# Kernel tuning notes

Hardware: AMD Instinct MI355X
Metric: run time of the kernel (lower is better)

Reference implementation:

```python
import jax, jax.numpy as jnp
import numpy as np

IN_SIZE = 64
NUM_FEATURES = 32
NUM_HEADS = 8
EPS = 1e-5


def setup_inputs() -> dict:
    key = jax.random.key(0)
    ks = jax.random.split(key, 12)
    D, F, Hh = IN_SIZE, NUM_FEATURES, NUM_HEADS
    M = Hh * F  # MLP width = num_heads * num_features
    s = 0.05
    return {
        "x": jax.random.normal(ks[0], (2, D, 48, 48), dtype=jnp.float32),
        # stacked per-head projection weights, stored [in, out]
        "Wq": jax.random.normal(ks[1], (Hh, D, F), dtype=jnp.float32) * s,
        "bq": jax.random.normal(ks[2], (Hh, F), dtype=jnp.float32) * s,
        "Wk": jax.random.normal(ks[3], (Hh, D, F), dtype=jnp.float32) * s,
        "bk": jax.random.normal(ks[4], (Hh, F), dtype=jnp.float32) * s,
        "Wv": jax.random.normal(ks[5], (Hh, D, F), dtype=jnp.float32) * s,
        "bv": jax.random.normal(ks[6], (Hh, F), dtype=jnp.float32) * s,
        "W1": jax.random.normal(ks[7], (M, M), dtype=jnp.float32) * s,
        "b1": jax.random.normal(ks[8], (M,), dtype=jnp.float32) * s,
        "W2": jax.random.normal(ks[9], (M, M), dtype=jnp.float32) * s,
        "b2": jax.random.normal(ks[10], (M,), dtype=jnp.float32) * s,
        "gamma": jnp.ones((M,), dtype=jnp.float32),
        "beta": jnp.zeros((M,), dtype=jnp.float32),
    }


def _inorm_lastdim(y):
    # InstanceNorm1d applied to channels-last tensor: normalizes LAST dim,
    # biased variance, eps=1e-5, no affine.
    mu = jnp.mean(y, axis=-1, keepdims=True)
    var = jnp.mean(jnp.square(y - mu), axis=-1, keepdims=True)
    return (y - mu) / jnp.sqrt(var + EPS)


def reference(x, Wq, bq, Wk, bk, Wv, bv, W1, b1, W2, b2, gamma, beta):
    N, D, H, W = x.shape
    F = NUM_FEATURES
    L = H * W
    flat = jnp.transpose(x, (0, 2, 3, 1)).reshape(N, L, D)  # [N, L, D]

    def proj(Wm, bm):  # Wm [Hh, D, F], bm [Hh, F] -> [Hh, N, L, F]
        y = jnp.einsum('nld,hdf->hnlf', flat, Wm) + bm[:, None, None, :]
        return jax.nn.relu(_inorm_lastdim(y))

    Q = proj(Wq, bq)
    K = proj(Wk, bk)
    V = proj(Wv, bv)

    scores = jnp.einsum('hnlf,hnmf->hnlm', Q, K) / jnp.sqrt(jnp.float32(F))
    # original: F.softmax(scaled) on 3D [N,L,L] -> legacy dim=1 (first L axis)
    att = jax.nn.softmax(scores, axis=2)
    A = jnp.einsum('hnlm,hnmf->hnlf', att, V)  # [Hh, N, L, F]

    heads = jnp.transpose(A, (1, 2, 0, 3)).reshape(N, L, NUM_HEADS * F)
    m = jax.nn.relu(heads @ W1 + b1)
    m = jax.nn.relu(m @ W2 + b2)
    o = _inorm_lastdim(m + heads)
    o = gamma * o + beta  # [N, L, Hh*F]
    return jnp.transpose(o, (0, 2, 1)).reshape(N, NUM_HEADS * F, H, W)
```

## Files before the change

kernel.cpp:

```cpp
#include <hip/hip_runtime.h>
#include <hip/hip_bf16.h>
#include <stdint.h>

#define L_TOT 2304
#define D_IN  64
#define NF    32
#define NH    8
#define NB    2
#define MW    256
#define CHS   8
#define NSTRIP (L_TOT/32)

constexpr float EPSV  = 1e-5f;
constexpr float SCALE2 = 0.2550351f;

typedef __bf16  bf16x8  __attribute__((ext_vector_type(8)));
typedef float   f32x16  __attribute__((ext_vector_type(16)));
typedef float   f32x4   __attribute__((ext_vector_type(4)));

union U32x4BF { uint32_t u[4]; bf16x8 v; };

static __device__ __forceinline__ uint32_t pack_bf16(float a, float b) {
    union { __bf16 h[2]; uint32_t u; } r;
    r.h[0] = (__bf16)a;
    r.h[1] = (__bf16)b;
    return r.u;
}

__global__ __launch_bounds__(256) void k_prep(
    const float* __restrict__ x,
    const float* __restrict__ Wq, const float* __restrict__ Wk, const float* __restrict__ Wv,
    const float* __restrict__ W1, const float* __restrict__ W2,
    __hip_bfloat16* __restrict__ xb, __hip_bfloat16* __restrict__ Wqkvt,
    __hip_bfloat16* __restrict__ W1t, __hip_bfloat16* __restrict__ W2t)
{
    const int job = blockIdx.x;
    const int tx = threadIdx.x & 31, ty = threadIdx.x >> 5;
    __shared__ float t[64][33];

    if (job < 128) {
        const int z = job >> 6;
        const int tt = job & 63;
        const int bi = (tt >> 3) * 32, bj = (tt & 7) * 32;
        const float* src = z ? W2 : W1;
        __hip_bfloat16* dst = z ? W2t : W1t;
        #pragma unroll
        for (int k = 0; k < 4; ++k)
            t[ty + 8 * k][tx] = src[(size_t)(bi + ty + 8 * k) * MW + bj + tx];
        __syncthreads();
        #pragma unroll
        for (int k = 0; k < 4; ++k)
            dst[(size_t)(bj + ty + 8 * k) * MW + bi + tx] =
                __float2bfloat16(t[tx][ty + 8 * k]);
        return;
    }

    const float* src;
    size_t sstride;
    __hip_bfloat16* dst;
    if (job < 152) {
        int j = job - 128;
        int mtx = j >> 3, h = j & 7;
        const float* Wm = mtx == 0 ? Wq : (mtx == 1 ? Wk : Wv);
        src = Wm + (size_t)h * D_IN * NF;
        sstride = NF;
        dst = Wqkvt + (size_t)j * NF * D_IN;
    } else {
        int i = job - 152;
        int n = i / NSTRIP, lt = i % NSTRIP;
        src = x + (size_t)n * D_IN * L_TOT + lt * 32;
        sstride = L_TOT;
        dst = xb + ((size_t)n * L_TOT + lt * 32) * D_IN;
    }
    #pragma unroll
    for (int k = 0; k < 8; ++k)
        t[ty + 8 * k][tx] = src[(size_t)(ty + 8 * k) * sstride + tx];
    __syncthreads();
    #pragma unroll
    for (int k = 0; k < 4; ++k) {
        int col = ty + 8 * k;
        #pragma unroll
        for (int j = 0; j < 2; ++j)
            dst[(size_t)col * D_IN + tx + 32 * j] = __float2bfloat16(t[tx + 32 * j][col]);
    }
}

__global__ __launch_bounds__(512) void k_proj(
    const __hip_bfloat16* __restrict__ xb, const __hip_bfloat16* __restrict__ Wqkvt,
    const float* __restrict__ bq, const float* __restrict__ bk, const float* __restrict__ bv,
    __hip_bfloat16* __restrict__ Qo, __hip_bfloat16* __restrict__ Ko,
    __hip_bfloat16* __restrict__ Vt)
{
    const int ltile = blockIdx.x;
    const int n = blockIdx.y;
    const int mtx = blockIdx.z;
    const int h = threadIdx.x >> 6;
    const int l0 = ltile * 32;
    const int lane = threadIdx.x & 63;
    const int c = lane & 31, hi = lane >> 5;
    const int hn = h * NB + n;

    const bf16x8* xp = reinterpret_cast<const bf16x8*>(
        xb + ((size_t)n * L_TOT + l0 + c) * D_IN);
    bf16x8 xf[4];
    #pragma unroll
    for (int t = 0; t < 4; ++t) xf[t] = xp[2 * t + hi];

    const float* bsp = mtx == 0 ? bq : (mtx == 1 ? bk : bv);

    const bf16x8* wp = reinterpret_cast<const bf16x8*>(
        Wqkvt + ((size_t)(mtx * NH + h) * NF + c) * D_IN);
    f32x16 acc = {};
    #pragma unroll
    for (int t = 0; t < 4; ++t)
        acc = __builtin_amdgcn_mfma_f32_32x32x16_bf16(wp[2 * t + hi], xf[t], acc, 0, 0, 0);

    float bb[16];
    #pragma unroll
    for (int g = 0; g < 4; ++g) {
        float4 t4 = *reinterpret_cast<const float4*>(&bsp[h * NF + 8 * g + 4 * hi]);
        bb[4 * g + 0] = t4.x; bb[4 * g + 1] = t4.y;
        bb[4 * g + 2] = t4.z; bb[4 * g + 3] = t4.w;
    }

    float v[16], s = 0.f, s2 = 0.f;
    #pragma unroll
    for (int r = 0; r < 16; ++r) {
        v[r] = acc[r] + bb[r];
        s += v[r]; s2 += v[r] * v[r];
    }
    s  += __shfl_xor(s, 32, 64);
    s2 += __shfl_xor(s2, 32, 64);
    float mu = s * (1.f / 32);
    float rstd = rsqrtf(s2 * (1.f / 32) - mu * mu + EPSV);
    float y[16];
    #pragma unroll
    for (int r = 0; r < 16; ++r) y[r] = fmaxf((v[r] - mu) * rstd, 0.f);

    if (mtx == 2) {
        #pragma unroll
        for (int r = 0; r < 16; ++r) {
            int f = (r & 3) + 8 * (r >> 2) + 4 * hi;
            Vt[((size_t)(hn * NSTRIP + ltile) * NF + f) * 32 + c] = __float2bfloat16(y[r]);
        }
    } else {
        if (mtx == 0) {
            #pragma unroll
            for (int r = 0; r < 16; ++r) y[r] *= SCALE2;
        }
        uint32_t pk[8];
        #pragma unroll
        for (int q = 0; q < 8; ++q) pk[q] = pack_bf16(y[2 * q], y[2 * q + 1]);
        uint32_t rr[4];
        #pragma unroll
        for (int j = 0; j < 4; ++j)
            rr[j] = (uint32_t)__shfl_xor((int)(hi ? pk[j] : pk[4 + j]), 32, 64);
        uint32_t row[8];
        if (hi == 0) {
            row[0] = pk[0]; row[1] = pk[1]; row[2] = rr[0]; row[3] = rr[1];
            row[4] = pk[2]; row[5] = pk[3]; row[6] = rr[2]; row[7] = rr[3];
        } else {
            row[0] = rr[0]; row[1] = rr[1]; row[2] = pk[4]; row[3] = pk[5];
            row[4] = rr[2]; row[5] = rr[3]; row[6] = pk[6]; row[7] = pk[7];
        }
        __hip_bfloat16* dst = (mtx == 0 ? Qo : Ko)
            + ((size_t)hn * L_TOT + l0 + c) * NF + hi * 16;
        reinterpret_cast<uint4*>(dst)[0] = make_uint4(row[0], row[1], row[2], row[3]);
        reinterpret_cast<uint4*>(dst)[1] = make_uint4(row[4], row[5], row[6], row[7]);
    }
}

__global__ __launch_bounds__(256) void k_stats(
    const __hip_bfloat16* __restrict__ Qb, const __hip_bfloat16* __restrict__ Kb,
    float* __restrict__ zpart)
{
    const int w = threadIdx.x >> 6;
    const int strip = blockIdx.x * 4 + w;
    const int hn = blockIdx.y;
    const int chunk = blockIdx.z;
    const int lane = threadIdx.x & 63;
    const int c = lane & 31, hi = lane >> 5;

    const bf16x8* kp = reinterpret_cast<const bf16x8*>(
        Kb + ((size_t)hn * L_TOT + strip * 32 + c) * NF);
    const bf16x8 kb0 = kp[hi];
    const bf16x8 kb1 = kp[2 + hi];

    float z0 = 0.f, z1 = 0.f, z2 = 0.f, z3 = 0.f;

    for (int it = 0; it < (L_TOT / 32) / CHS; ++it) {
        const int l0 = (chunk * ((L_TOT / 32) / CHS) + it) * 32;
        const bf16x8* qp = reinterpret_cast<const bf16x8*>(
            Qb + ((size_t)hn * L_TOT + l0 + c) * NF);
        f32x16 s16 = {};
        s16 = __builtin_amdgcn_mfma_f32_32x32x16_bf16(qp[hi], kb0, s16, 0, 0, 0);
        s16 = __builtin_amdgcn_mfma_f32_32x32x16_bf16(qp[2 + hi], kb1, s16, 0, 0, 0);
        #pragma unroll
        for (int r = 0; r < 4; ++r) z0 += exp2f(s16[r]);
        #pragma unroll
        for (int r = 4; r < 8; ++r) z1 += exp2f(s16[r]);
        #pragma unroll
        for (int r = 8; r < 12; ++r) z2 += exp2f(s16[r]);
        #pragma unroll
        for (int r = 12; r < 16; ++r) z3 += exp2f(s16[r]);
    }
    float Z = (z0 + z1) + (z2 + z3);
    Z += __shfl_xor(Z, 32, 64);
    if (hi == 0)
        zpart[((size_t)chunk * 16 + hn) * L_TOT + strip * 32 + c] = Z;
}

__global__ __launch_bounds__(256) void k_norm(
    const float* __restrict__ zpart, __hip_bfloat16* __restrict__ Vt)
{
    const int strip = blockIdx.x, hn = blockIdx.y;
    __shared__ float zs[CHS][32];
    __shared__ float zinv_s[32];

    const int cc = threadIdx.x >> 5, p = threadIdx.x & 31;
    zs[cc][p] = zpart[((size_t)cc * 16 + hn) * L_TOT + strip * 32 + p];
    __syncthreads();
    if (threadIdx.x < 32) {
        float Z = 0.f;
        #pragma unroll
        for (int k = 0; k < CHS; ++k) Z += zs[k][threadIdx.x];
        zinv_s[threadIdx.x] = 1.f / Z;
    }
    __syncthreads();

    const int f = threadIdx.x >> 3, mg = (threadIdx.x & 7) * 4;
    __hip_bfloat16* pv = Vt + ((size_t)(hn * NSTRIP + strip) * NF + f) * 32 + mg;
    uint2* p2v = reinterpret_cast<uint2*>(pv);
    union { uint2 u2; __bf16 h[4]; } in, outv;
    in.u2 = *p2v;
    outv.h[0] = (__bf16)((float)in.h[0] * zinv_s[mg + 0]);
    outv.h[1] = (__bf16)((float)in.h[1] * zinv_s[mg + 1]);
    outv.h[2] = (__bf16)((float)in.h[2] * zinv_s[mg + 2]);
    outv.h[3] = (__bf16)((float)in.h[3] * zinv_s[mg + 3]);
    *p2v = outv.u2;
}

static __device__ __forceinline__ void apply_strip(
    int st, int hn, const bf16x8& qb0, const bf16x8& qb1,
    const __hip_bfloat16* __restrict__ Kb, const __hip_bfloat16* __restrict__ Vt,
    int c, int hi, f32x16& acc)
{
    const bf16x8* kp = reinterpret_cast<const bf16x8*>(
        Kb + ((size_t)hn * L_TOT + st * 32 + c) * NF);
    f32x16 s16 = {};
    s16 = __builtin_amdgcn_mfma_f32_32x32x16_bf16(kp[hi], qb0, s16, 0, 0, 0);
    s16 = __builtin_amdgcn_mfma_f32_32x32x16_bf16(kp[2 + hi], qb1, s16, 0, 0, 0);

    float p[16];
    #pragma unroll
    for (int r = 0; r < 16; ++r) p[r] = exp2f(s16[r]);

    uint32_t wp[8];
    #pragma unroll
    for (int q = 0; q < 8; ++q) wp[q] = pack_bf16(p[2 * q], p[2 * q + 1]);

    uint32_t sendA = hi ? wp[0] : wp[2];
    uint32_t sendB = hi ? wp[1] : wp[3];
    uint32_t rA = (uint32_t)__shfl_xor((int)sendA, 32, 64);
    uint32_t rB = (uint32_t)__shfl_xor((int)sendB, 32, 64);
    U32x4BF fragP0;
    fragP0.u[0] = hi ? rA    : wp[0];
    fragP0.u[1] = hi ? rB    : wp[1];
    fragP0.u[2] = hi ? wp[2] : rA;
    fragP0.u[3] = hi ? wp[3] : rB;
    uint32_t sendC = hi ? wp[4] : wp[6];
    uint32_t sendD = hi ? wp[5] : wp[7];
    uint32_t rC = (uint32_t)__shfl_xor((int)sendC, 32, 64);
    uint32_t rD = (uint32_t)__shfl_xor((int)sendD, 32, 64);
    U32x4BF fragP1;
    fragP1.u[0] = hi ? rC    : wp[4];
    fragP1.u[1] = hi ? rD    : wp[5];
    fragP1.u[2] = hi ? wp[6] : rC;
    fragP1.u[3] = hi ? wp[7] : rD;

    const bf16x8* vp = reinterpret_cast<const bf16x8*>(
        Vt + ((size_t)(hn * NSTRIP + st) * NF + c) * 32);
    acc = __builtin_amdgcn_mfma_f32_32x32x16_bf16(fragP0.v, vp[hi], acc, 0, 0, 0);
    acc = __builtin_amdgcn_mfma_f32_32x32x16_bf16(fragP1.v, vp[2 + hi], acc, 0, 0, 0);
}

__global__ __launch_bounds__(512) void k_apply(
    const __hip_bfloat16* __restrict__ Qb, const __hip_bfloat16* __restrict__ Kb,
    const __hip_bfloat16* __restrict__ Vt,
    float* __restrict__ partA)
{
    const int w = threadIdx.x >> 6;
    const int ltile = blockIdx.x;
    const int l0 = ltile * 32;
    const int hn = blockIdx.y;
    const int lane = threadIdx.x & 63;
    const int c = lane & 31, hi = lane >> 5;

    const bf16x8* qp = reinterpret_cast<const bf16x8*>(
        Qb + ((size_t)hn * L_TOT + l0 + c) * NF);
    const bf16x8 qb0 = qp[hi];
    const bf16x8 qb1 = qp[2 + hi];

    f32x16 accA = {}, accB = {};
    const int sbase = w * (NSTRIP / 8);
    #pragma unroll
    for (int it2 = 0; it2 < 4; ++it2) {
        apply_strip(sbase + 2 * it2,     hn, qb0, qb1, Kb, Vt, c, hi, accA);
        apply_strip(sbase + 2 * it2 + 1, hn, qb0, qb1, Kb, Vt, c, hi, accB);
    }
    apply_strip(sbase + 8, hn, qb0, qb1, Kb, Vt, c, hi, accA);

    __shared__ float red[8][16][64];
    #pragma unroll
    for (int r = 0; r < 16; ++r) red[w][r][lane] = accA[r] + accB[r];
    __syncthreads();

    const int n = hn & 1, h = hn >> 1;
    float* outp = partA + ((size_t)(n * L_TOT + l0)) * MW + h * NF + c;
    #pragma unroll
    for (int j = 0; j < 2; ++j) {
        const int r = 2 * w + j;
        float sv = 0.f;
        #pragma unroll
        for (int k = 0; k < 8; ++k) sv += red[k][r][lane];
        const int row = (r & 3) + 8 * (r >> 2) + 4 * hi;
        outp[(size_t)row * MW] = sv;
    }
}

__global__ __launch_bounds__(512) void k_mlp(
    const float* __restrict__ partA,
    const __hip_bfloat16* __restrict__ W1t, const float* __restrict__ b1,
    const __hip_bfloat16* __restrict__ W2t, const float* __restrict__ b2,
    const float* __restrict__ gamma, const float* __restrict__ beta,
    float* __restrict__ out)
{
    const int blk = blockIdx.x;
    const int n  = blk / (L_TOT / 16);
    const int l0 = (blk % (L_TOT / 16)) * 16;
    const int tid = threadIdx.x;
    const int w = tid >> 6, lane = tid & 63;
    const int ar = lane & 15;
    const int kg = lane >> 4;
    const int n0 = w * 32;

    __shared__ __align__(16) char smem[50176];
    float (*hsf)[MW] = reinterpret_cast<float (*)[MW]>(smem);
    __hip_bfloat16 (*hA)[264]  = reinterpret_cast<__hip_bfloat16 (*)[264]>(smem + 16384);
    __hip_bfloat16 (*msb)[264] = reinterpret_cast<__hip_bfloat16 (*)[264]>(smem + 24832);
    float (*ys)[MW] = reinterpret_cast<float (*)[MW]>(smem + 33280);
    float (*rs)[4]  = reinterpret_cast<float (*)[4]>(smem + 49664);
    float (*rs2)[4] = reinterpret_cast<float (*)[4]>(smem + 49920);

    for (int idx = tid; idx < 16 * MW; idx += 512) {
        int r = idx >> 8, i = idx & 255;
        float v = partA[((size_t)n * L_TOT + l0 + r) * MW + i];
        hsf[r][i] = v;
        hA[r][i] = __float2bfloat16(v);
    }
    __syncthreads();

    f32x4 acc0 = {}, acc1 = {};
    {
        const __hip_bfloat16* B0p = W1t + (size_t)(n0 + ar) * MW + kg * 8;
        const __hip_bfloat16* B1p = W1t + (size_t)(n0 + 16 + ar) * MW + kg * 8;
        #pragma unroll
        for (int ks = 0; ks < 8; ++ks) {
            bf16x8 a  = *reinterpret_cast<const bf16x8*>(&hA[ar][ks * 32 + kg * 8]);
            bf16x8 b0 = *reinterpret_cast<const bf16x8*>(B0p + ks * 32);
            bf16x8 b1v = *reinterpret_cast<const bf16x8*>(B1p + ks * 32);
            acc0 = __builtin_amdgcn_mfma_f32_16x16x32_bf16(a, b0, acc0, 0, 0, 0);
            acc1 = __builtin_amdgcn_mfma_f32_16x16x32_bf16(a, b1v, acc1, 0, 0, 0);
        }
    }
    {
        const float bb0 = b1[n0 + ar], bb1 = b1[n0 + 16 + ar];
        #pragma unroll
        for (int r = 0; r < 4; ++r) {
            int row = kg * 4 + r;
            msb[row][n0 + ar]      = __float2bfloat16(fmaxf(acc0[r] + bb0, 0.f));
            msb[row][n0 + 16 + ar] = __float2bfloat16(fmaxf(acc1[r] + bb1, 0.f));
        }
    }
    __syncthreads();

    f32x4 a20 = {}, a21 = {};
    {
        const __hip_bfloat16* B0p = W2t + (size_t)(n0 + ar) * MW + kg * 8;
        const __hip_bfloat16* B1p = W2t + (size_t)(n0 + 16 + ar) * MW + kg * 8;
        #pragma unroll
        for (int ks = 0; ks < 8; ++ks) {
            bf16x8 a  = *reinterpret_cast<const bf16x8*>(&msb[ar][ks * 32 + kg * 8]);
            bf16x8 b0 = *reinterpret_cast<const bf16x8*>(B0p + ks * 32);
            bf16x8 b1v = *reinterpret_cast<const bf16x8*>(B1p + ks * 32);
            a20 = __builtin_amdgcn_mfma_f32_16x16x32_bf16(a, b0, a20, 0, 0, 0);
            a21 = __builtin_amdgcn_mfma_f32_16x16x32_bf16(a, b1v, a21, 0, 0, 0);
        }
    }
    {
        const float bb0 = b2[n0 + ar], bb1 = b2[n0 + 16 + ar];
        #pragma unroll
        for (int r = 0; r < 4; ++r) {
            int row = kg * 4 + r;
            ys[row][n0 + ar]      = fmaxf(a20[r] + bb0, 0.f) + hsf[row][n0 + ar];
            ys[row][n0 + 16 + ar] = fmaxf(a21[r] + bb1, 0.f) + hsf[row][n0 + 16 + ar];
        }
    }
    __syncthreads();

    const int col = tid & 255;
    const int half = tid >> 8;
    const int wid = (tid >> 6) & 3;
    float vv[8];
    #pragma unroll
    for (int r = 0; r < 8; ++r) {
        float v = ys[half * 8 + r][col];
        vv[r] = v;
        float s = v, s2 = v * v;
        #pragma unroll
        for (int o = 32; o >= 1; o >>= 1) { s += __shfl_xor(s, o, 64); s2 += __shfl_xor(s2, o, 64); }
        if (lane == 0) { rs[half * 8 + r][wid] = s; rs2[half * 8 + r][wid] = s2; }
    }
    __syncthreads();
    const float g = gamma[col], be = beta[col];
    float ov[8];
    #pragma unroll
    for (int r = 0; r < 8; ++r) {
        int row = half * 8 + r;
        float s  = rs[row][0]  + rs[row][1]  + rs[row][2]  + rs[row][3];
        float s2 = rs2[row][0] + rs2[row][1] + rs2[row][2] + rs2[row][3];
        float mu  = s  * (1.f / MW);
        float var = s2 * (1.f / MW) - mu * mu;
        ov[r] = g * ((vv[r] - mu) * rsqrtf(var + EPSV)) + be;
    }
    float* ob = out + ((size_t)n * MW + col) * L_TOT + l0 + half * 8;
    reinterpret_cast<float4*>(ob)[0] = make_float4(ov[0], ov[1], ov[2], ov[3]);
    reinterpret_cast<float4*>(ob)[1] = make_float4(ov[4], ov[5], ov[6], ov[7]);
}

extern "C" void kernel_launch(void* const* d_in, const int* in_sizes, int n_in,
                              void* d_out, int out_size, void* d_ws, size_t ws_size,
                              hipStream_t stream) {
    const float* x  = (const float*)d_in[0];
    const float* Wq = (const float*)d_in[1];
    const float* bq = (const float*)d_in[2];
    const float* Wk = (const float*)d_in[3];
    const float* bk = (const float*)d_in[4];
    const float* Wv = (const float*)d_in[5];
    const float* bv = (const float*)d_in[6];
    const float* W1 = (const float*)d_in[7];
    const float* b1 = (const float*)d_in[8];
    const float* W2 = (const float*)d_in[9];
    const float* b2 = (const float*)d_in[10];
    const float* gm = (const float*)d_in[11];
    const float* bt = (const float*)d_in[12];
    float* out = (float*)d_out;

    const size_t QKVE = (size_t)16 * L_TOT * NF;
    const size_t XBE  = (size_t)NB * L_TOT * D_IN;
    const size_t WQE  = (size_t)3 * NH * NF * D_IN;
    const size_t WTE  = (size_t)MW * MW;
    const size_t ZN = (size_t)CHS * 16 * L_TOT;

    __hip_bfloat16* Qb = (__hip_bfloat16*)d_ws;
    __hip_bfloat16* Kb = Qb + QKVE;
    __hip_bfloat16* Vt = Kb + QKVE;
    __hip_bfloat16* xb = Vt + QKVE;
    __hip_bfloat16* Wqkvt = xb + XBE;
    __hip_bfloat16* W1t = Wqkvt + WQE;
    __hip_bfloat16* W2t = W1t + WTE;
    float* zpart = (float*)(W2t + WTE);
    float* partA = zpart + ZN;

    k_prep<<<dim3(296), dim3(256), 0, stream>>>(
        x, Wq, Wk, Wv, W1, W2, xb, Wqkvt, W1t, W2t);
    k_proj<<<dim3(NSTRIP, NB, 3), dim3(512), 0, stream>>>(
        xb, Wqkvt, bq, bk, bv, Qb, Kb, Vt);
    k_stats<<<dim3(NSTRIP / 4, 16, CHS), dim3(256), 0, stream>>>(Qb, Kb, zpart);
    k_norm<<<dim3(NSTRIP, 16), dim3(256), 0, stream>>>(zpart, Vt);
    k_apply<<<dim3(NSTRIP, 16), dim3(512), 0, stream>>>(Qb, Kb, Vt, partA);
    k_mlp<<<dim3(NB * (L_TOT / 16)), dim3(512), 0, stream>>>(
        partA, W1t, b1, W2t, b2, gm, bt, out);
}
```

Measured before the change: 122.5 us.

## Fuse softmax normalization into stats via atomic counter; double query tile in apply

Removes the separate k_norm launch. The last k_stats block to finish each strip group, found with an atomic counter that k_prep zeroes, sums the partial Z values and rescales V in place. k_apply now handles two 32-row query tiles per block, reusing each loaded K/V fragment for both and halving the grid. This trades a kernel launch and repeated K/V loads for atomics, thread fences, fewer blocks and higher register pressure.

New measurement: 298.0 us. 2.43x slower.

```diff
diff --git a/kernel.cpp b/kernel.cpp
--- a/kernel.cpp
+++ b/kernel.cpp
@@ -32,11 +32,15 @@
     const float* __restrict__ Wq, const float* __restrict__ Wk, const float* __restrict__ Wv,
     const float* __restrict__ W1, const float* __restrict__ W2,
     __hip_bfloat16* __restrict__ xb, __hip_bfloat16* __restrict__ Wqkvt,
-    __hip_bfloat16* __restrict__ W1t, __hip_bfloat16* __restrict__ W2t)
+    __hip_bfloat16* __restrict__ W1t, __hip_bfloat16* __restrict__ W2t,
+    unsigned int* __restrict__ cnt)
 {
     const int job = blockIdx.x;
     const int tx = threadIdx.x & 31, ty = threadIdx.x >> 5;
     __shared__ float t[64][33];
+
+    if (threadIdx.x == 0 && job < 16 * (NSTRIP / 4))
+        cnt[job] = 0u;
 
     if (job < 128) {
         const int z = job >> 6;
@@ -172,7 +176,8 @@
 
 __global__ __launch_bounds__(256) void k_stats(
     const __hip_bfloat16* __restrict__ Qb, const __hip_bfloat16* __restrict__ Kb,
-    float* __restrict__ zpart)
+    float* __restrict__ zpart, __hip_bfloat16* __restrict__ Vt,
+    unsigned int* __restrict__ cnt)
 {
     const int w = threadIdx.x >> 6;
     const int strip = blockIdx.x * 4 + w;
@@ -208,49 +213,44 @@
     Z += __shfl_xor(Z, 32, 64);
     if (hi == 0)
         zpart[((size_t)chunk * 16 + hn) * L_TOT + strip * 32 + c] = Z;
-}
-
-__global__ __launch_bounds__(256) void k_norm(
-    const float* __restrict__ zpart, __hip_bfloat16* __restrict__ Vt)
+
+    __shared__ unsigned int done;
+    __shared__ float zi[4][32];
+    __threadfence();
+    __syncthreads();
+    if (threadIdx.x == 0)
+        done = atomicAdd(&cnt[hn * (NSTRIP / 4) + blockIdx.x], 1u);
+    __syncthreads();
+    if (done == CHS - 1) {
+        __threadfence();
+        const int sid = threadIdx.x >> 6, ln = threadIdx.x & 63;
+        const int strip2 = blockIdx.x * 4 + sid;
+        if (ln < 32) {
+            float Zs = 0.f;
+            #pragma unroll
+            for (int k = 0; k < CHS; ++k)
+                Zs += zpart[((size_t)k * 16 + hn) * L_TOT + strip2 * 32 + ln];
+            zi[sid][ln] = 1.f / Zs;
+        }
+        __syncthreads();
+        const int f = ln >> 1, mh = (ln & 1) * 16;
+        __hip_bfloat16* pv = Vt + ((size_t)(hn * NSTRIP + strip2) * NF + f) * 32 + mh;
+        uint4* p4 = reinterpret_cast<uint4*>(pv);
+        #pragma unroll
+        for (int g = 0; g < 2; ++g) {
+            union { uint4 u4; __bf16 h[8]; } in, outv;
+            in.u4 = p4[g];
+            #pragma unroll
+            for (int e = 0; e < 8; ++e)
+                outv.h[e] = (__bf16)((float)in.h[e] * zi[sid][mh + g * 8 + e]);
+            p4[g] = outv.u4;
+        }
+    }
+}
+
+static __device__ __forceinline__ void make_pfrags(
+    const f32x16& s16, int hi, U32x4BF& fragP0, U32x4BF& fragP1)
 {
-    const int strip = blockIdx.x, hn = blockIdx.y;
-    __shared__ float zs[CHS][32];
-    __shared__ float zinv_s[32];
-
-    const int cc = threadIdx.x >> 5, p = threadIdx.x & 31;
-    zs[cc][p] = zpart[((size_t)cc * 16 + hn) * L_TOT + strip * 32 + p];
-    __syncthreads();
-    if (threadIdx.x < 32) {
-        float Z = 0.f;
-        #pragma unroll
-        for (int k = 0; k < CHS; ++k) Z += zs[k][threadIdx.x];
-        zinv_s[threadIdx.x] = 1.f / Z;
-    }
-    __syncthreads();
-
-    const int f = threadIdx.x >> 3, mg = (threadIdx.x & 7) * 4;
-    __hip_bfloat16* pv = Vt + ((size_t)(hn * NSTRIP + strip) * NF + f) * 32 + mg;
-    uint2* p2v = reinterpret_cast<uint2*>(pv);
-    union { uint2 u2; __bf16 h[4]; } in, outv;
-    in.u2 = *p2v;
-    outv.h[0] = (__bf16)((float)in.h[0] * zinv_s[mg + 0]);
-    outv.h[1] = (__bf16)((float)in.h[1] * zinv_s[mg + 1]);
-    outv.h[2] = (__bf16)((float)in.h[2] * zinv_s[mg + 2]);
-    outv.h[3] = (__bf16)((float)in.h[3] * zinv_s[mg + 3]);
-    *p2v = outv.u2;
-}
-
-static __device__ __forceinline__ void apply_strip(
-    int st, int hn, const bf16x8& qb0, const bf16x8& qb1,
-    const __hip_bfloat16* __restrict__ Kb, const __hip_bfloat16* __restrict__ Vt,
-    int c, int hi, f32x16& acc)
-{
-    const bf16x8* kp = reinterpret_cast<const bf16x8*>(
-        Kb + ((size_t)hn * L_TOT + st * 32 + c) * NF);
-    f32x16 s16 = {};
-    s16 = __builtin_amdgcn_mfma_f32_32x32x16_bf16(kp[hi], qb0, s16, 0, 0, 0);
-    s16 = __builtin_amdgcn_mfma_f32_32x32x16_bf16(kp[2 + hi], qb1, s16, 0, 0, 0);
-
     float p[16];
     #pragma unroll
     for (int r = 0; r < 16; ++r) p[r] = exp2f(s16[r]);
@@ -263,7 +263,6 @@
     uint32_t sendB = hi ? wp[1] : wp[3];
     uint32_t rA = (uint32_t)__shfl_xor((int)sendA, 32, 64);
     uint32_t rB = (uint32_t)__shfl_xor((int)sendB, 32, 64);
-    U32x4BF fragP0;
     fragP0.u[0] = hi ? rA    : wp[0];
     fragP0.u[1] = hi ? rB    : wp[1];
     fragP0.u[2] = hi ? wp[2] : rA;
@@ -272,16 +271,10 @@
     uint32_t sendD = hi ? wp[5] : wp[7];
     uint32_t rC = (uint32_t)__shfl_xor((int)sendC, 32, 64);
     uint32_t rD = (uint32_t)__shfl_xor((int)sendD, 32, 64);
-    U32x4BF fragP1;
     fragP1.u[0] = hi ? rC    : wp[4];
     fragP1.u[1] = hi ? rD    : wp[5];
     fragP1.u[2] = hi ? wp[6] : rC;
     fragP1.u[3] = hi ? wp[7] : rD;
-
-    const bf16x8* vp = reinterpret_cast<const bf16x8*>(
-        Vt + ((size_t)(hn * NSTRIP + st) * NF + c) * 32);
-    acc = __builtin_amdgcn_mfma_f32_32x32x16_bf16(fragP0.v, vp[hi], acc, 0, 0, 0);
-    acc = __builtin_amdgcn_mfma_f32_32x32x16_bf16(fragP1.v, vp[2 + hi], acc, 0, 0, 0);
 }
 
 __global__ __launch_bounds__(512) void k_apply(
@@ -290,41 +283,83 @@
     float* __restrict__ partA)
 {
     const int w = threadIdx.x >> 6;
-    const int ltile = blockIdx.x;
-    const int l0 = ltile * 32;
+    const int l0 = blockIdx.x * 64;
     const int hn = blockIdx.y;
     const int lane = threadIdx.x & 63;
     const int c = lane & 31, hi = lane >> 5;
 
-    const bf16x8* qp = reinterpret_cast<const bf16x8*>(
+    const bf16x8* qp0 = reinterpret_cast<const bf16x8*>(
         Qb + ((size_t)hn * L_TOT + l0 + c) * NF);
-    const bf16x8 qb0 = qp[hi];
-    const bf16x8 qb1 = qp[2 + hi];
-
-    f32x16 accA = {}, accB = {};
-    const int sbase = w * (NSTRIP / 8);
-    #pragma unroll
-    for (int it2 = 0; it2 < 4; ++it2) {
-        apply_strip(sbase + 2 * it2,     hn, qb0, qb1, Kb, Vt, c, hi, accA);
-        apply_strip(sbase + 2 * it2 + 1, hn, qb0, qb1, Kb, Vt, c, hi, accB);
-    }
-    apply_strip(sbase + 8, hn, qb0, qb1, Kb, Vt, c, hi, accA);
+    const bf16x8* qp1 = reinterpret_cast<const bf16x8*>(
+        Qb + ((size_t)hn * L_TOT + l0 + 32 + c) * NF);
+    const bf16x8 qa0 = qp0[hi], qa1 = qp0[2 + hi];
+    const bf16x8 qc0 = qp1[hi], qc1 = qp1[2 + hi];
+
+    f32x16 acc0 = {}, acc1 = {};
+
+    #pragma unroll 3
+    for (int it = 0; it < NSTRIP / 8; ++it) {
+        const int st = w * (NSTRIP / 8) + it;
+        const bf16x8* kp = reinterpret_cast<const bf16x8*>(
+            Kb + ((size_t)hn * L_TOT + st * 32 + c) * NF);
+        const bf16x8 kf0 = kp[hi], kf1 = kp[2 + hi];
+        const bf16x8* vp = reinterpret_cast<const bf16x8*>(
+            Vt + ((size_t)(hn * NSTRIP + st) * NF + c) * 32);
+        const bf16x8 vf0 = vp[hi], vf1 = vp[2 + hi];
+
+        {
+            f32x16 s16 = {};
+            s16 = __builtin_amdgcn_mfma_f32_32x32x16_bf16(kf0, qa0, s16, 0, 0, 0);
+            s16 = __builtin_amdgcn_mfma_f32_32x32x16_bf16(kf1, qa1, s16, 0, 0, 0);
+            U32x4BF fragP0, fragP1;
+            make_pfrags(s16, hi, fragP0, fragP1);
+            acc0 = __builtin_amdgcn_mfma_f32_32x32x16_bf16(fragP0.v, vf0, acc0, 0, 0, 0);
+            acc0 = __builtin_amdgcn_mfma_f32_32x32x16_bf16(fragP1.v, vf1, acc0, 0, 0, 0);
+        }
+        {
+            f32x16 s16 = {};
+            s16 = __builtin_amdgcn_mfma_f32_32x32x16_bf16(kf0, qc0, s16, 0, 0, 0);
+            s16 = __builtin_amdgcn_mfma_f32_32x32x16_bf16(kf1, qc1, s16, 0, 0, 0);
+            U32x4BF fragP0, fragP1;
+            make_pfrags(s16, hi, fragP0, fragP1);
+            acc1 = __builtin_amdgcn_mfma_f32_32x32x16_bf16(fragP0.v, vf0, acc1, 0, 0, 0);
+            acc1 = __builtin_amdgcn_mfma_f32_32x32x16_bf16(fragP1.v, vf1, acc1, 0, 0, 0);
+        }
+    }
 
     __shared__ float red[8][16][64];
-    #pragma unroll
-    for (int r = 0; r < 16; ++r) red[w][r][lane] = accA[r] + accB[r];
-    __syncthreads();
-
     const int n = hn & 1, h = hn >> 1;
-    float* outp = partA + ((size_t)(n * L_TOT + l0)) * MW + h * NF + c;
-    #pragma unroll
-    for (int j = 0; j < 2; ++j) {
-        const int r = 2 * w + j;
-        float sv = 0.f;
-        #pragma unroll
-        for (int k = 0; k < 8; ++k) sv += red[k][r][lane];
-        const int row = (r & 3) + 8 * (r >> 2) + 4 * hi;
-        outp[(size_t)row * MW] = sv;
+
+    #pragma unroll
+    for (int r = 0; r < 16; ++r) red[w][r][lane] = acc0[r];
+    __syncthreads();
+    {
+        float* outp = partA + ((size_t)(n * L_TOT + l0)) * MW + h * NF + c;
+        #pragma unroll
+        for (int j = 0; j < 2; ++j) {
+            const int r = 2 * w + j;
+            float sv = 0.f;
+            #pragma unroll
+            for (int k = 0; k < 8; ++k) sv += red[k][r][lane];
+            const int row = (r & 3) + 8 * (r >> 2) + 4 * hi;
+            outp[(size_t)row * MW] = sv;
+        }
+    }
+    __syncthreads();
+    #pragma unroll
+    for (int r = 0; r < 16; ++r) red[w][r][lane] = acc1[r];
+    __syncthreads();
+    {
+        float* outp = partA + ((size_t)(n * L_TOT + l0 + 32)) * MW + h * NF + c;
+        #pragma unroll
+        for (int j = 0; j < 2; ++j) {
+            const int r = 2 * w + j;
+            float sv = 0.f;
+            #pragma unroll
+            for (int k = 0; k < 8; ++k) sv += red[k][r][lane];
+            const int row = (r & 3) + 8 * (r >> 2) + 4 * hi;
+            outp[(size_t)row * MW] = sv;
+        }
     }
 }
 
@@ -461,6 +496,7 @@
     const size_t WQE  = (size_t)3 * NH * NF * D_IN;
     const size_t WTE  = (size_t)MW * MW;
     const size_t ZN = (size_t)CHS * 16 * L_TOT;
+    const size_t PAN = (size_t)NB * L_TOT * MW;
 
     __hip_bfloat16* Qb = (__hip_bfloat16*)d_ws;
     __hip_bfloat16* Kb = Qb + QKVE;
@@ -471,14 +507,15 @@
     __hip_bfloat16* W2t = W1t + WTE;
     float* zpart = (float*)(W2t + WTE);
     float* partA = zpart + ZN;
+    unsigned int* cnt = (unsigned int*)(partA + PAN);
 
     k_prep<<<dim3(296), dim3(256), 0, stream>>>(
-        x, Wq, Wk, Wv, W1, W2, xb, Wqkvt, W1t, W2t);
+        x, Wq, Wk, Wv, W1, W2, xb, Wqkvt, W1t, W2t, cnt);
     k_proj<<<dim3(NSTRIP, NB, 3), dim3(512), 0, stream>>>(
         xb, Wqkvt, bq, bk, bv, Qb, Kb, Vt);
-    k_stats<<<dim3(NSTRIP / 4, 16, CHS), dim3(256), 0, stream>>>(Qb, Kb, zpart);
-    k_norm<<<dim3(NSTRIP, 16), dim3(256), 0, stream>>>(zpart, Vt);
-    k_apply<<<dim3(NSTRIP, 16), dim3(512), 0, stream>>>(Qb, Kb, Vt, partA);
+    k_stats<<<dim3(NSTRIP / 4, 16, CHS), dim3(256), 0, stream>>>(
+        Qb, Kb, zpart, Vt, cnt);
+    k_apply<<<dim3(NSTRIP / 2, 16), dim3(512), 0, stream>>>(Qb, Kb, Vt, partA);
     k_mlp<<<dim3(NB * (L_TOT / 16)), dim3(512), 0, stream>>>(
         partA, W1t, b1, W2t, b2, gm, bt, out);
 }
```
